# Kernel tuning notes

Hardware: AMD Instinct MI355X
Metric: run time of the kernel (lower is better)

Reference implementation:

```python
import jax, jax.numpy as jnp
import numpy as np

B, S, D_MODEL, D_QK = 4, 4096, 256, 64


def setup_inputs() -> dict:
    key = jax.random.key(0)
    ks = jax.random.split(key, 6)
    enc_q = jax.random.normal(ks[0], (B, S, D_MODEL), dtype=jnp.float32)
    enc_k = jax.random.normal(ks[1], (B, S, D_MODEL), dtype=jnp.float32)
    enc_v = jax.random.normal(ks[2], (B, S, D_MODEL), dtype=jnp.float32)
    # torch nn.Linear weight layout: [out_features, in_features]
    Wq = jax.random.normal(ks[3], (D_QK, D_MODEL), dtype=jnp.float32) * (D_MODEL ** -0.5)
    Wk = jax.random.normal(ks[4], (D_QK, D_MODEL), dtype=jnp.float32) * (D_MODEL ** -0.5)
    Wv = jax.random.normal(ks[5], (D_MODEL, D_MODEL), dtype=jnp.float32) * (D_MODEL ** -0.5)
    # causal mask: True above the diagonal -> masked out (matches masked_fill semantics)
    mask = jnp.triu(jnp.ones((S, S), dtype=jnp.bool_), k=1)
    return {"encodings_for_q": enc_q, "encodings_for_k": enc_k,
            "encodings_for_v": enc_v, "mask": mask,
            "Wq": Wq, "Wk": Wk, "Wv": Wv}


def reference(encodings_for_q, encodings_for_k, encodings_for_v, mask, Wq, Wk, Wv):
    # linear projections (no bias): x @ W.T
    q = jnp.einsum('bsd,qd->bsq', encodings_for_q, Wq)   # [B,S,d_qk]
    k = jnp.einsum('bsd,qd->bsq', encodings_for_k, Wk)   # [B,S,d_qk]
    v = jnp.einsum('bsd,ed->bse', encodings_for_v, Wv)   # [B,S,d_model]
    scale = k.shape[-1] ** 0.5                            # sqrt(d_qk)
    sims = jnp.einsum('bsq,btq->bst', q, k) / scale       # [B,S,S]
    sims = jnp.where(mask, jnp.float32(-1e9), sims)
    attn = jax.nn.softmax(sims, axis=-1)
    return jnp.einsum('bst,bte->bse', attn, v)            # [B,S,d_model]
```

## Files before the change

kernel.cpp:

```cpp
#include <hip/hip_runtime.h>


#define BATCH 4
#define SEQ   4096
#define DM    256
#define DQK   64

typedef __bf16 bf16x8 __attribute__((ext_vector_type(8)));
typedef __bf16 bf16x2 __attribute__((ext_vector_type(2)));
typedef float  f32x16 __attribute__((ext_vector_type(16)));

__device__ __forceinline__ unsigned short f2bf(float f) {
    __bf16 h = (__bf16)f;
    return __builtin_bit_cast(unsigned short, h);
}
__device__ __forceinline__ unsigned int pk2bf(float lo, float hi) {
    bf16x2 v = {(__bf16)lo, (__bf16)hi};
    return __builtin_bit_cast(unsigned int, v);
}
__device__ __forceinline__ bf16x8 u4bf(uint4 u) { return __builtin_bit_cast(bf16x8, u); }

__device__ __forceinline__ void repack_store(const f32x16& acc, int q2, int l,
                                             uint4* __restrict__ out, size_t tile_ofs_u4) {
    unsigned int d0[4], d1[4], p0[4], p1[4];
#pragma unroll
    for (int h = 0; h < 4; ++h) {
        d0[h] = pk2bf(acc[4*h + 0], acc[4*h + 1]);
        d1[h] = pk2bf(acc[4*h + 2], acc[4*h + 3]);
        p0[h] = __shfl_xor((int)d0[h], 32);
        p1[h] = __shfl_xor((int)d1[h], 32);
    }
#pragma unroll
    for (int kc = 0; kc < 2; ++kc) {
        int h = 2*kc + q2;
        uint4 v = (q2 == 0) ? make_uint4(d0[h], d1[h], p0[h], p1[h])
                            : make_uint4(p0[h], p1[h], d0[h], d1[h]);
        out[tile_ofs_u4 + (size_t)kc * 64 + l] = v;
    }
}

__device__ __forceinline__ int obase(int T) {
    return (T < 24) ? (T - 12) : 12 + (T - 24) * 2;
}
__device__ __forceinline__ int dbase(int T) {
    return (T < 24) ? (T - 12) * 2 : 24 + (T - 24) * 3;
}

__global__ __launch_bounds__(256) void proj(const float* __restrict__ Xq,
                                            const float* __restrict__ Xk,
                                            const float* __restrict__ Xv,
                                            const float* __restrict__ Wq,
                                            const float* __restrict__ Wk,
                                            const float* __restrict__ Wv,
                                            uint4* __restrict__ qf,
                                            uint4* __restrict__ kf,
                                            uint4* __restrict__ vf) {
    __shared__ unsigned short Xs[64][264];
    __shared__ unsigned short Ws[64][264];

    const int z = blockIdx.z;
    const int bx = blockIdx.x, b = blockIdx.y;
    const float* X = (z == 0) ? Xq : (z == 1) ? Xk : Xv;
    const float* W = (z == 0) ? Wq : (z == 1) ? Wk : Wv;
    const int s0 = bx * 64;
    const int tid = threadIdx.x, w = tid >> 6, l = tid & 63, ln = l & 31, q2 = l >> 5;

#pragma unroll
    for (int i = 0; i < 16; ++i) {
        int f = i * 256 + tid;
        int r = f >> 6, c4 = f & 63;
        float4 xv = *(const float4*)&X[((size_t)b * SEQ + s0 + r) * DM + c4 * 4];
        ushort4 h; h.x = f2bf(xv.x); h.y = f2bf(xv.y); h.z = f2bf(xv.z); h.w = f2bf(xv.w);
        *(ushort4*)&Xs[r][c4 * 4] = h;
    }

    if (z < 2) {
#pragma unroll
        for (int i = 0; i < 16; ++i) {
            int f = i * 256 + tid;
            int r = f >> 6, c4 = f & 63;
            float4 wv = *(const float4*)&W[(size_t)r * DM + c4 * 4];
            ushort4 h; h.x = f2bf(wv.x); h.y = f2bf(wv.y); h.z = f2bf(wv.z); h.w = f2bf(wv.w);
            *(ushort4*)&Ws[r][c4 * 4] = h;
        }
        __syncthreads();
        const int msub = w >> 1, nsub = w & 1;
        f32x16 a0 = {}, a1 = {};
#pragma unroll
        for (int c = 0; c < 16; c += 2) {
            bf16x8 af0 = u4bf(*(const uint4*)&Ws[msub*32 + ln][c*16 + q2*8]);
            bf16x8 bf0 = u4bf(*(const uint4*)&Xs[nsub*32 + ln][c*16 + q2*8]);
            a0 = __builtin_amdgcn_mfma_f32_32x32x16_bf16(af0, bf0, a0, 0, 0, 0);
            bf16x8 af1 = u4bf(*(const uint4*)&Ws[msub*32 + ln][(c+1)*16 + q2*8]);
            bf16x8 bf1 = u4bf(*(const uint4*)&Xs[nsub*32 + ln][(c+1)*16 + q2*8]);
            a1 = __builtin_amdgcn_mfma_f32_32x32x16_bf16(af1, bf1, a1, 0, 0, 0);
        }
        f32x16 acc = a0 + a1;
        size_t base = (((size_t)(b*128 + bx*2 + nsub)) * 4 + 2*msub) * 64;
        repack_store(acc, q2, l, (z == 0) ? qf : kf, base);
    } else {
        const int msub = w & 1, nsub = w >> 1;
        for (int ec = 0; ec < 4; ++ec) {
            __syncthreads();
#pragma unroll
            for (int i = 0; i < 16; ++i) {
                int f = i * 256 + tid;
                int r = f >> 6, c4 = f & 63;
                float4 wv = *(const float4*)&W[(size_t)(ec*64 + r) * DM + c4 * 4];
                ushort4 h; h.x = f2bf(wv.x); h.y = f2bf(wv.y); h.z = f2bf(wv.z); h.w = f2bf(wv.w);
                *(ushort4*)&Ws[r][c4 * 4] = h;
            }
            __syncthreads();
            f32x16 a0 = {}, a1 = {};
#pragma unroll
            for (int c = 0; c < 16; c += 2) {
                bf16x8 af0 = u4bf(*(const uint4*)&Xs[msub*32 + ln][c*16 + q2*8]);
                bf16x8 bf0 = u4bf(*(const uint4*)&Ws[nsub*32 + ln][c*16 + q2*8]);
                a0 = __builtin_amdgcn_mfma_f32_32x32x16_bf16(af0, bf0, a0, 0, 0, 0);
                bf16x8 af1 = u4bf(*(const uint4*)&Xs[msub*32 + ln][(c+1)*16 + q2*8]);
                bf16x8 bf1 = u4bf(*(const uint4*)&Ws[nsub*32 + ln][(c+1)*16 + q2*8]);
                a1 = __builtin_amdgcn_mfma_f32_32x32x16_bf16(af1, bf1, a1, 0, 0, 0);
            }
            f32x16 acc = a0 + a1;
            int et = ec*2 + nsub;
            size_t base = (((size_t)(b*8 + et)) * 256 + (size_t)bx*4 + msub*2) * 64;
            repack_store(acc, q2, l, vf, base);
        }
    }
}

__global__ __launch_bounds__(512, 2) void attn(const uint4* __restrict__ qf,
                                               const uint4* __restrict__ kf,
                                               const uint4* __restrict__ vf,
                                               float* __restrict__ out,
                                               unsigned short* __restrict__ Op,
                                               float* __restrict__ Dp) {
    __shared__ uint4 Pb[2][2][8][64];
    __shared__ float denp[4][2][64];
    __shared__ float dfin[64];

    const int bid = blockIdx.x;
    const int slot = bid & 7;
    const int b = slot >> 1, qh = slot & 1;
    const int task = bid >> 3;
    int T, cc, nc;
    if (task < 12)      { T = task;                cc = 0;               nc = 1; }
    else if (task < 36) { int q = task - 12; T = 12 + (q >> 1); cc = q & 1;       nc = 2; }
    else                { int q = task - 36; T = 24 + q / 3;    cc = q - 3*(q/3); nc = 3; }
    const int n = T + 1;
    const int j0 = cc * n / nc, j1 = (cc + 1) * n / nc;

    const int tid = threadIdx.x, w = tid >> 6, l = tid & 63, ln = l & 31, q2 = l >> 5;
    const int ks = w & 3, qg = w >> 2;
    const int qsub = qh * 2 + qg;
    const int et = w;
    const float cfac = 0.18033688011112042f;

    bf16x8 qv[4];
#pragma unroll
    for (int c = 0; c < 4; ++c)
        qv[c] = u4bf(qf[(((size_t)b*128 + T*4 + qsub) * 4 + c) * 64 + l]);

    f32x16 oa[2] = {};
    float den = 0.f;

    const uint4* kp = kf + (((size_t)b*128 + j0*4 + ks) * 4) * 64 + l;
    uint4 kaf[4];
#pragma unroll
    for (int c = 0; c < 4; ++c) kaf[c] = kp[c * 64];

    uint4 vbs[8];
    {
        const uint4* vp = vf + (((size_t)b*8 + et) * 256 + (size_t)j0*8) * 64 + l;
#pragma unroll
        for (int kc = 0; kc < 8; ++kc) vbs[kc] = vp[kc * 64];
    }
    const uint4* vpnA = vf + (((size_t)b*8 + et) * 256 + (size_t)(j0+1)*8) * 64 + l;
    const uint4* vpnB = vpnA + 256;

    const int jend = (j1 == T + 1) ? T : j1;

    for (int jt = j0; jt < jend; ++jt) {
        const int buf = jt & 1;

        f32x16 s = {};
#pragma unroll
        for (int c = 0; c < 4; ++c)
            s = __builtin_amdgcn_mfma_f32_32x32x16_bf16(u4bf(kaf[c]), qv[c], s, 0, 0, 0);

        float pv[16], pd = 0.f;
#pragma unroll
        for (int r = 0; r < 16; ++r) {
            float e = __builtin_exp2f(s[r] * cfac);
            pv[r] = e; pd += e;
        }
        den += pd;
#pragma unroll
        for (int quad = 0; quad < 4; ++quad) {
            unsigned int lo = pk2bf(pv[4*quad + 0], pv[4*quad + 1]);
            unsigned int hi = pk2bf(pv[4*quad + 2], pv[4*quad + 3]);
            int kcg = ks*2 + (quad >> 1);
            int h   = quad & 1;
            char* dst = (char*)&Pb[buf][qg][kcg][h*32 + ln] + q2*8;
            *(uint2*)dst = make_uint2(lo, hi);
        }
        __syncthreads();

        kp += 1024;
#pragma unroll
        for (int c = 0; c < 4; ++c) kaf[c] = kp[c * 64];

#pragma unroll
        for (int kc = 0; kc < 8; ++kc) {
            bf16x8 vb = u4bf(vbs[kc]);
            vbs[kc] = (kc < 4) ? vpnA[kc * 64] : vpnB[(kc - 4) * 64];
#pragma unroll
            for (int qsl = 0; qsl < 2; ++qsl) {
                bf16x8 pa = u4bf(Pb[buf][qsl][kc][l]);
                oa[qsl] = __builtin_amdgcn_mfma_f32_32x32x16_bf16(pa, vb, oa[qsl], 0, 0, 0);
            }
        }
        vpnA += 512; vpnB += 512;
    }

    if (j1 == T + 1) {
        const int buf = T & 1;
        f32x16 s = {};
#pragma unroll
        for (int c = 0; c < 4; ++c)
            s = __builtin_amdgcn_mfma_f32_32x32x16_bf16(u4bf(kaf[c]), qv[c], s, 0, 0, 0);

        float pv[16], pd = 0.f;
#pragma unroll
        for (int r = 0; r < 16; ++r) {
            float e = __builtin_exp2f(s[r] * cfac);
            int klocal = 4*q2 + (r & 3) + 8*(r >> 2);
            if (ks*32 + klocal > qsub*32 + ln) e = 0.f;
            pv[r] = e; pd += e;
        }
        den += pd;
#pragma unroll
        for (int quad = 0; quad < 4; ++quad) {
            unsigned int lo = pk2bf(pv[4*quad + 0], pv[4*quad + 1]);
            unsigned int hi = pk2bf(pv[4*quad + 2], pv[4*quad + 3]);
            int kcg = ks*2 + (quad >> 1);
            int h   = quad & 1;
            char* dst = (char*)&Pb[buf][qg][kcg][h*32 + ln] + q2*8;
            *(uint2*)dst = make_uint2(lo, hi);
        }
        __syncthreads();
#pragma unroll
        for (int kc = 0; kc < 8; ++kc) {
            bf16x8 vb = u4bf(vbs[kc]);
#pragma unroll
            for (int qsl = 0; qsl < 2; ++qsl) {
                bf16x8 pa = u4bf(Pb[buf][qsl][kc][l]);
                oa[qsl] = __builtin_amdgcn_mfma_f32_32x32x16_bf16(pa, vb, oa[qsl], 0, 0, 0);
            }
        }
    }

    denp[ks][qg][l] = den;
    __syncthreads();
    if (tid < 64) {
        int qgl = tid >> 5, qln = tid & 31;
        float sden = 0.f;
#pragma unroll
        for (int p = 0; p < 4; ++p)
#pragma unroll
            for (int hh = 0; hh < 2; ++hh)
                sden += denp[p][qgl][hh*32 + qln];
        dfin[tid] = (nc == 1) ? 1.0f / sden : sden;
    }
    __syncthreads();

    if (nc == 1) {
#pragma unroll
        for (int qsl = 0; qsl < 2; ++qsl)
#pragma unroll
            for (int r = 0; r < 16; ++r) {
                int qrow = qsl*32 + (r & 3) + 8*(r >> 2) + 4*q2;
                out[((size_t)b*SEQ + T*128 + qh*64 + qrow) * DM + et*32 + ln] = oa[qsl][r] * dfin[qrow];
            }
    } else if (cc == 0) {
#pragma unroll
        for (int qsl = 0; qsl < 2; ++qsl)
#pragma unroll
            for (int r = 0; r < 16; ++r) {
                int qrow = qsl*32 + (r & 3) + 8*(r >> 2) + 4*q2;
                out[((size_t)b*SEQ + T*128 + qh*64 + qrow) * DM + et*32 + ln] = oa[qsl][r];
            }
        if (tid < 64) Dp[((size_t)b*48 + dbase(T)) * 128 + qh*64 + tid] = dfin[tid];
    } else {
        size_t pidx = (size_t)b*28 + obase(T) + (cc - 1);
#pragma unroll
        for (int qsl = 0; qsl < 2; ++qsl)
#pragma unroll
            for (int r = 0; r < 16; ++r) {
                int qrow = qsl*32 + (r & 3) + 8*(r >> 2) + 4*q2;
                Op[(pidx*128 + qh*64 + qrow) * DM + et*32 + ln] = f2bf(oa[qsl][r]);
            }
        if (tid < 64) Dp[((size_t)b*48 + dbase(T) + cc) * 128 + qh*64 + tid] = dfin[tid];
    }
}

__global__ __launch_bounds__(256) void combine(const unsigned short* __restrict__ Op,
                                               const float* __restrict__ Dp,
                                               float* __restrict__ out) {
    const int T = 12 + blockIdx.x, b = blockIdx.y, qq = blockIdx.z;
    const int nc = (T < 24) ? 2 : 3;
    const int t = threadIdx.x;
    const size_t db = (size_t)b*48 + dbase(T);
    const size_t pb = (size_t)b*28 + obase(T);
#pragma unroll 4
    for (int r = 0; r < 32; ++r) {
        int q = qq*32 + r;
        size_t oofs = ((size_t)b*SEQ + T*128 + q) * DM + t;
        float sum = out[oofs];
        float dsum = 0.f;
        for (int c = 0; c < nc; ++c) dsum += Dp[(db + c)*128 + q];
        for (int c = 1; c < nc; ++c) {
            unsigned int uv = Op[((pb + c - 1)*128 + q) * DM + t];
            sum += __builtin_bit_cast(float, uv << 16);
        }
        out[oofs] = sum / dsum;
    }
}

extern "C" void kernel_launch(void* const* d_in, const int* in_sizes, int n_in,
                              void* d_out, int out_size, void* d_ws, size_t ws_size,
                              hipStream_t stream) {
    const float* enc_q = (const float*)d_in[0];
    const float* enc_k = (const float*)d_in[1];
    const float* enc_v = (const float*)d_in[2];
    const float* Wq = (const float*)d_in[4];
    const float* Wk = (const float*)d_in[5];
    const float* Wv = (const float*)d_in[6];
    float* out = (float*)d_out;

    uint4* qf = (uint4*)d_ws;
    uint4* kf = qf + 131072;
    uint4* vf = kf + 131072;
    unsigned short* Op = (unsigned short*)(vf + 524288);
    float* Dp = (float*)(Op + (size_t)4*28*128*256);

    proj<<<dim3(64, 4, 3), 256, 0, stream>>>(enc_q, enc_k, enc_v, Wq, Wk, Wv, qf, kf, vf);
    attn<<<480, 512, 0, stream>>>(qf, kf, vf, out, Op, Dp);
    combine<<<dim3(20, 4, 4), 256, 0, stream>>>(Op, Dp, out);
}
```

Measured before the change: 210.6 us.

## Process two key tiles per iteration with quad-buffered P to halve barriers

The attention loop now computes scores and softmax numerators for two key tiles before a single __syncthreads, using four P buffers in LDS instead of two. K fragments for both tiles are prefetched into registers, and the diagonal mask is applied conditionally inside the unified loop instead of in a separate tail. This halves the block-wide barriers and gives more independent MFMA/exp work between syncs. The cost is more VGPRs for the second K fragment set and doubled P-buffer LDS, which could raise spills under the 512x2 launch bounds.

```diff
diff --git a/kernel.cpp b/kernel.cpp
--- a/kernel.cpp
+++ b/kernel.cpp
@@ -135,7 +135,7 @@
                                                float* __restrict__ out,
                                                unsigned short* __restrict__ Op,
                                                float* __restrict__ Dp) {
-    __shared__ uint4 Pb[2][2][8][64];
+    __shared__ uint4 Pb[4][2][8][64];
     __shared__ float denp[4][2][64];
     __shared__ float dfin[64];
 
@@ -164,34 +164,134 @@
     f32x16 oa[2] = {};
     float den = 0.f;
 
-    const uint4* kp = kf + (((size_t)b*128 + j0*4 + ks) * 4) * 64 + l;
-    uint4 kaf[4];
-#pragma unroll
-    for (int c = 0; c < 4; ++c) kaf[c] = kp[c * 64];
-
+    uint4 kaf0[4], kaf1[4];
+    {
+        const int jp1 = (j0 + 1 < j1) ? j0 + 1 : j0;
+#pragma unroll
+        for (int c = 0; c < 4; ++c) {
+            kaf0[c] = kf[(((size_t)b*128 + j0*4 + ks) * 4 + c) * 64 + l];
+            kaf1[c] = kf[(((size_t)b*128 + jp1*4 + ks) * 4 + c) * 64 + l];
+        }
+    }
+    const size_t vbase = ((size_t)b*8 + et) * 256;
     uint4 vbs[8];
-    {
-        const uint4* vp = vf + (((size_t)b*8 + et) * 256 + (size_t)j0*8) * 64 + l;
-#pragma unroll
-        for (int kc = 0; kc < 8; ++kc) vbs[kc] = vp[kc * 64];
-    }
-    const uint4* vpnA = vf + (((size_t)b*8 + et) * 256 + (size_t)(j0+1)*8) * 64 + l;
-    const uint4* vpnB = vpnA + 256;
-
-    const int jend = (j1 == T + 1) ? T : j1;
-
-    for (int jt = j0; jt < jend; ++jt) {
-        const int buf = jt & 1;
-
+#pragma unroll
+    for (int kc = 0; kc < 8; ++kc)
+        vbs[kc] = vf[(vbase + (size_t)j0*8 + kc) * 64 + l];
+
+    const int jpe = j0 + ((j1 - j0) & ~1);
+    int pp = 0;
+
+    for (int jt = j0; jt < jpe; jt += 2, pp ^= 1) {
+        const int bA = 2*pp, bB = 2*pp + 1;
+
+        {
+            f32x16 s = {};
+#pragma unroll
+            for (int c = 0; c < 4; ++c)
+                s = __builtin_amdgcn_mfma_f32_32x32x16_bf16(u4bf(kaf0[c]), qv[c], s, 0, 0, 0);
+            const bool diag = (jt == T);
+            float pv[16], pd = 0.f;
+#pragma unroll
+            for (int r = 0; r < 16; ++r) {
+                float e = __builtin_exp2f(s[r] * cfac);
+                if (diag) {
+                    int klocal = 4*q2 + (r & 3) + 8*(r >> 2);
+                    if (ks*32 + klocal > qsub*32 + ln) e = 0.f;
+                }
+                pv[r] = e; pd += e;
+            }
+            den += pd;
+#pragma unroll
+            for (int quad = 0; quad < 4; ++quad) {
+                unsigned int lo = pk2bf(pv[4*quad + 0], pv[4*quad + 1]);
+                unsigned int hi = pk2bf(pv[4*quad + 2], pv[4*quad + 3]);
+                int kcg = ks*2 + (quad >> 1);
+                int h   = quad & 1;
+                char* dst = (char*)&Pb[bA][qg][kcg][h*32 + ln] + q2*8;
+                *(uint2*)dst = make_uint2(lo, hi);
+            }
+        }
+        {
+            f32x16 s = {};
+#pragma unroll
+            for (int c = 0; c < 4; ++c)
+                s = __builtin_amdgcn_mfma_f32_32x32x16_bf16(u4bf(kaf1[c]), qv[c], s, 0, 0, 0);
+            const bool diag = (jt + 1 == T);
+            float pv[16], pd = 0.f;
+#pragma unroll
+            for (int r = 0; r < 16; ++r) {
+                float e = __builtin_exp2f(s[r] * cfac);
+                if (diag) {
+                    int klocal = 4*q2 + (r & 3) + 8*(r >> 2);
+                    if (ks*32 + klocal > qsub*32 + ln) e = 0.f;
+                }
+                pv[r] = e; pd += e;
+            }
+            den += pd;
+#pragma unroll
+            for (int quad = 0; quad < 4; ++quad) {
+                unsigned int lo = pk2bf(pv[4*quad + 0], pv[4*quad + 1]);
+                unsigned int hi = pk2bf(pv[4*quad + 2], pv[4*quad + 3]);
+                int kcg = ks*2 + (quad >> 1);
+                int h   = quad & 1;
+                char* dst = (char*)&Pb[bB][qg][kcg][h*32 + ln] + q2*8;
+                *(uint2*)dst = make_uint2(lo, hi);
+            }
+        }
+        __syncthreads();
+
+        {
+            const int jk0 = (jt + 2 < j1) ? jt + 2 : j1 - 1;
+            const int jk1 = (jt + 3 < j1) ? jt + 3 : j1 - 1;
+#pragma unroll
+            for (int c = 0; c < 4; ++c) {
+                kaf0[c] = kf[(((size_t)b*128 + jk0*4 + ks) * 4 + c) * 64 + l];
+                kaf1[c] = kf[(((size_t)b*128 + jk1*4 + ks) * 4 + c) * 64 + l];
+            }
+        }
+
+#pragma unroll
+        for (int kc = 0; kc < 8; ++kc) {
+            bf16x8 vb = u4bf(vbs[kc]);
+            vbs[kc] = vf[(vbase + (size_t)(jt+1)*8 + kc) * 64 + l];
+#pragma unroll
+            for (int qsl = 0; qsl < 2; ++qsl) {
+                bf16x8 pa = u4bf(Pb[bA][qsl][kc][l]);
+                oa[qsl] = __builtin_amdgcn_mfma_f32_32x32x16_bf16(pa, vb, oa[qsl], 0, 0, 0);
+            }
+        }
+        {
+            const int jn2 = (jt + 2 < j1) ? jt + 2 : j1 - 1;
+#pragma unroll
+            for (int kc = 0; kc < 8; ++kc) {
+                bf16x8 vb = u4bf(vbs[kc]);
+                vbs[kc] = vf[(vbase + (size_t)jn2*8 + kc) * 64 + l];
+#pragma unroll
+                for (int qsl = 0; qsl < 2; ++qsl) {
+                    bf16x8 pa = u4bf(Pb[bB][qsl][kc][l]);
+                    oa[qsl] = __builtin_amdgcn_mfma_f32_32x32x16_bf16(pa, vb, oa[qsl], 0, 0, 0);
+                }
+            }
+        }
+    }
+
+    if (jpe < j1) {
+        const int jt = j1 - 1;
+        const int bA = 2*pp;
         f32x16 s = {};
 #pragma unroll
         for (int c = 0; c < 4; ++c)
-            s = __builtin_amdgcn_mfma_f32_32x32x16_bf16(u4bf(kaf[c]), qv[c], s, 0, 0, 0);
-
+            s = __builtin_amdgcn_mfma_f32_32x32x16_bf16(u4bf(kaf0[c]), qv[c], s, 0, 0, 0);
+        const bool diag = (jt == T);
         float pv[16], pd = 0.f;
 #pragma unroll
         for (int r = 0; r < 16; ++r) {
             float e = __builtin_exp2f(s[r] * cfac);
+            if (diag) {
+                int klocal = 4*q2 + (r & 3) + 8*(r >> 2);
+                if (ks*32 + klocal > qsub*32 + ln) e = 0.f;
+            }
             pv[r] = e; pd += e;
         }
         den += pd;
@@ -201,60 +301,16 @@
             unsigned int hi = pk2bf(pv[4*quad + 2], pv[4*quad + 3]);
             int kcg = ks*2 + (quad >> 1);
             int h   = quad & 1;
-            char* dst = (char*)&Pb[buf][qg][kcg][h*32 + ln] + q2*8;
+            char* dst = (char*)&Pb[bA][qg][kcg][h*32 + ln] + q2*8;
             *(uint2*)dst = make_uint2(lo, hi);
         }
         __syncthreads();
-
-        kp += 1024;
-#pragma unroll
-        for (int c = 0; c < 4; ++c) kaf[c] = kp[c * 64];
-
 #pragma unroll
         for (int kc = 0; kc < 8; ++kc) {
             bf16x8 vb = u4bf(vbs[kc]);
-            vbs[kc] = (kc < 4) ? vpnA[kc * 64] : vpnB[(kc - 4) * 64];
 #pragma unroll
             for (int qsl = 0; qsl < 2; ++qsl) {
-                bf16x8 pa = u4bf(Pb[buf][qsl][kc][l]);
-                oa[qsl] = __builtin_amdgcn_mfma_f32_32x32x16_bf16(pa, vb, oa[qsl], 0, 0, 0);
-            }
-        }
-        vpnA += 512; vpnB += 512;
-    }
-
-    if (j1 == T + 1) {
-        const int buf = T & 1;
-        f32x16 s = {};
-#pragma unroll
-        for (int c = 0; c < 4; ++c)
-            s = __builtin_amdgcn_mfma_f32_32x32x16_bf16(u4bf(kaf[c]), qv[c], s, 0, 0, 0);
-
-        float pv[16], pd = 0.f;
-#pragma unroll
-        for (int r = 0; r < 16; ++r) {
-            float e = __builtin_exp2f(s[r] * cfac);
-            int klocal = 4*q2 + (r & 3) + 8*(r >> 2);
-            if (ks*32 + klocal > qsub*32 + ln) e = 0.f;
-            pv[r] = e; pd += e;
-        }
-        den += pd;
-#pragma unroll
-        for (int quad = 0; quad < 4; ++quad) {
-            unsigned int lo = pk2bf(pv[4*quad + 0], pv[4*quad + 1]);
-            unsigned int hi = pk2bf(pv[4*quad + 2], pv[4*quad + 3]);
-            int kcg = ks*2 + (quad >> 1);
-            int h   = quad & 1;
-            char* dst = (char*)&Pb[buf][qg][kcg][h*32 + ln] + q2*8;
-            *(uint2*)dst = make_uint2(lo, hi);
-        }
-        __syncthreads();
-#pragma unroll
-        for (int kc = 0; kc < 8; ++kc) {
-            bf16x8 vb = u4bf(vbs[kc]);
-#pragma unroll
-            for (int qsl = 0; qsl < 2; ++qsl) {
-                bf16x8 pa = u4bf(Pb[buf][qsl][kc][l]);
+                bf16x8 pa = u4bf(Pb[bA][qsl][kc][l]);
                 oa[qsl] = __builtin_amdgcn_mfma_f32_32x32x16_bf16(pa, vb, oa[qsl], 0, 0, 0);
             }
         }
```

Result: faster. 205.5 us (-2.5%).
